# Kernel optimization log

Hardware: AMD Instinct MI355X
Metric: run time of the kernel (lower is better)

Reference implementation:

```python
import jax, jax.numpy as jnp
import numpy as np

B, L, D = 32, 1024, 128

def setup_inputs() -> dict:
    key = jax.random.key(0)
    kq, kk, kv, ks = jax.random.split(key, 4)
    Q = jax.random.normal(kq, (B, L, D), dtype=jnp.float32)
    K = jax.random.normal(kk, (B, L, D), dtype=jnp.float32)
    V = jax.random.normal(kv, (B, L, D), dtype=jnp.float32)
    kg_sim = jax.random.uniform(ks, (B, L, L), dtype=jnp.float32)
    scale = jnp.float32(1.0 / np.sqrt(D))
    return {"Q": Q, "K": K, "V": V, "scale": scale, "kg_sim": kg_sim}

def reference(Q, K, V, scale, kg_sim):
    # attention = -1 * (Q @ K^T) * scale   [B, L, L]
    attn = -scale * jnp.einsum('bqd,bkd->bqk', Q, K)
    # attention = -softmax(attention, axis=-1)
    attn = -jax.nn.softmax(attn, axis=-1)
    # beta = softmax(attention * kg_sim, axis=-1)
    beta = jax.nn.softmax(attn * kg_sim, axis=-1)
    # context = beta @ V   [B, L, D]
    return jnp.einsum('bqk,bkd->bqd', beta, V)
```

## Files before the change

kernel.cpp:

```cpp
#include <hip/hip_runtime.h>
#include <hip/hip_bf16.h>

#define L 1024
#define D 128
#define NB 32
#define BQ 16

typedef __attribute__((ext_vector_type(8))) short short8;
typedef __attribute__((ext_vector_type(4))) short short4v;
typedef __attribute__((ext_vector_type(4))) float f32x4;

__device__ __forceinline__ unsigned short f2bf(float f) {
    union { float f; unsigned int u; } x; x.f = f;
    unsigned int r = x.u + 0x7FFF + ((x.u >> 16) & 1);
    return (unsigned short)(r >> 16);
}
__device__ __forceinline__ float bf2f(unsigned short u) {
    union { unsigned int u; float f; } x; x.u = ((unsigned int)u) << 16;
    return x.f;
}

__global__ void vt_kernel(const float* __restrict__ V, unsigned short* __restrict__ Vt) {
    __shared__ unsigned short t[32][40];
    int id = blockIdx.x;
    int b = id >> 7;
    int rest = id & 127;
    int kt = rest >> 2, dt = rest & 3;
    int k0 = kt * 32, d0 = dt * 32;
    int tid = threadIdx.x;

    int kl = tid >> 3, dl4 = (tid & 7) * 4;
    const float* src = V + (((size_t)b * L + (k0 + kl)) * D) + d0 + dl4;
    float4 v = *(const float4*)src;
    t[dl4 + 0][kl] = f2bf(v.x);
    t[dl4 + 1][kl] = f2bf(v.y);
    t[dl4 + 2][kl] = f2bf(v.z);
    t[dl4 + 3][kl] = f2bf(v.w);
    __syncthreads();

    int dl = tid >> 3, kl4 = (tid & 7) * 4;
    unsigned short* dst = Vt + (((size_t)b * D + (d0 + dl)) * L) + k0 + kl4;
    short4v o;
    o[0] = (short)t[dl][kl4 + 0];
    o[1] = (short)t[dl][kl4 + 1];
    o[2] = (short)t[dl][kl4 + 2];
    o[3] = (short)t[dl][kl4 + 3];
    *(short4v*)dst = o;
}

__global__ __launch_bounds__(256, 4)
void attn_kernel(const float* __restrict__ Q, const float* __restrict__ K,
                 const float* __restrict__ scale_p, const float* __restrict__ kg,
                 const unsigned short* __restrict__ Vt, float* __restrict__ out) {
    __shared__ unsigned short S16[BQ * 1032];
    __shared__ unsigned short QL[BQ * 136];
    __shared__ float row_scale[BQ];

    const int tid = threadIdx.x;
    const int b  = blockIdx.x >> 6;
    const int q0 = (blockIdx.x & 63) * BQ;
    const float nsc = -scale_p[0];

    {
        int row = tid >> 4;
        int c8  = (tid & 15) * 8;
        const float* qp = Q + (((size_t)b * L) + q0 + row) * D + c8;
        float4 v0 = *(const float4*)qp;
        float4 v1 = *(const float4*)(qp + 4);
        unsigned short* dst = &QL[row * 136 + c8];
        dst[0] = f2bf(v0.x * nsc); dst[1] = f2bf(v0.y * nsc);
        dst[2] = f2bf(v0.z * nsc); dst[3] = f2bf(v0.w * nsc);
        dst[4] = f2bf(v1.x * nsc); dst[5] = f2bf(v1.y * nsc);
        dst[6] = f2bf(v1.z * nsc); dst[7] = f2bf(v1.w * nsc);
    }
    __syncthreads();

    const int wave = tid >> 6, lane = tid & 63;
    const int lr = lane & 15;
    const int lg = lane >> 4;

    short8 aq[4];
#pragma unroll
    for (int kb = 0; kb < 4; kb++)
        aq[kb] = *(const short8*)&QL[lr * 136 + kb * 32 + lg * 8];

    for (int ct = wave; ct < 64; ct += 4) {
        const float* kp = K + (((size_t)b * L) + ct * 16 + lr) * D + lg * 8;
        f32x4 acc = {0.f, 0.f, 0.f, 0.f};
#pragma unroll
        for (int kb = 0; kb < 4; kb++) {
            float4 x0 = *(const float4*)(kp + kb * 32);
            float4 x1 = *(const float4*)(kp + kb * 32 + 4);
            short8 bf;
            bf[0] = (short)f2bf(x0.x); bf[1] = (short)f2bf(x0.y);
            bf[2] = (short)f2bf(x0.z); bf[3] = (short)f2bf(x0.w);
            bf[4] = (short)f2bf(x1.x); bf[5] = (short)f2bf(x1.y);
            bf[6] = (short)f2bf(x1.z); bf[7] = (short)f2bf(x1.w);
            acc = __builtin_amdgcn_mfma_f32_16x16x32_bf16(aq[kb], bf, acc, 0, 0, 0);
        }
#pragma unroll
        for (int r = 0; r < 4; r++)
            S16[(lg * 4 + r) * 1032 + ct * 16 + lr] = f2bf(acc[r]);
    }
    __syncthreads();

    const int row = tid >> 4, l = tid & 15;
    unsigned short* srow = &S16[row * 1032];

    float m1 = -3.4e38f;
#pragma unroll 4
    for (int j = 0; j < 16; j++) {
        short4v v = *(const short4v*)&srow[l * 4 + 64 * j];
        float a0 = bf2f((unsigned short)v[0]), a1 = bf2f((unsigned short)v[1]);
        float a2 = bf2f((unsigned short)v[2]), a3 = bf2f((unsigned short)v[3]);
        m1 = fmaxf(m1, fmaxf(fmaxf(a0, a1), fmaxf(a2, a3)));
    }
#pragma unroll
    for (int m = 1; m < 16; m <<= 1) m1 = fmaxf(m1, __shfl_xor(m1, m, 64));

    float z1 = 0.f;
#pragma unroll 4
    for (int j = 0; j < 16; j++) {
        unsigned short* p = &srow[l * 4 + 64 * j];
        short4v v = *(const short4v*)p;
        float e0 = __expf(bf2f((unsigned short)v[0]) - m1);
        float e1 = __expf(bf2f((unsigned short)v[1]) - m1);
        float e2 = __expf(bf2f((unsigned short)v[2]) - m1);
        float e3 = __expf(bf2f((unsigned short)v[3]) - m1);
        z1 += (e0 + e1) + (e2 + e3);
        short4v o; o[0] = (short)f2bf(e0); o[1] = (short)f2bf(e1);
        o[2] = (short)f2bf(e2); o[3] = (short)f2bf(e3);
        *(short4v*)p = o;
    }
#pragma unroll
    for (int m = 1; m < 16; m <<= 1) z1 += __shfl_xor(z1, m, 64);
    const float iz1 = 1.0f / z1;

    const float* kgrow = kg + (((size_t)b * L) + q0 + row) * L;
    float m2 = -3.4e38f;
#pragma unroll 4
    for (int j = 0; j < 16; j++) {
        int c = l * 4 + 64 * j;
        float4 g = *(const float4*)&kgrow[c];
        unsigned short* p = &srow[c];
        short4v v = *(const short4v*)p;
        float t0 = -(bf2f((unsigned short)v[0]) * iz1) * g.x;
        float t1 = -(bf2f((unsigned short)v[1]) * iz1) * g.y;
        float t2 = -(bf2f((unsigned short)v[2]) * iz1) * g.z;
        float t3 = -(bf2f((unsigned short)v[3]) * iz1) * g.w;
        m2 = fmaxf(m2, fmaxf(fmaxf(t0, t1), fmaxf(t2, t3)));
        short4v o; o[0] = (short)f2bf(t0); o[1] = (short)f2bf(t1);
        o[2] = (short)f2bf(t2); o[3] = (short)f2bf(t3);
        *(short4v*)p = o;
    }
#pragma unroll
    for (int m = 1; m < 16; m <<= 1) m2 = fmaxf(m2, __shfl_xor(m2, m, 64));

    float z2 = 0.f;
#pragma unroll 4
    for (int j = 0; j < 16; j++) {
        unsigned short* p = &srow[l * 4 + 64 * j];
        short4v v = *(const short4v*)p;
        float e0 = __expf(bf2f((unsigned short)v[0]) - m2);
        float e1 = __expf(bf2f((unsigned short)v[1]) - m2);
        float e2 = __expf(bf2f((unsigned short)v[2]) - m2);
        float e3 = __expf(bf2f((unsigned short)v[3]) - m2);
        z2 += (e0 + e1) + (e2 + e3);
        short4v o; o[0] = (short)f2bf(e0); o[1] = (short)f2bf(e1);
        o[2] = (short)f2bf(e2); o[3] = (short)f2bf(e3);
        *(short4v*)p = o;
    }
#pragma unroll
    for (int m = 1; m < 16; m <<= 1) z2 += __shfl_xor(z2, m, 64);
    if (l == 0) row_scale[row] = 1.0f / z2;
    __syncthreads();

    const int dt0 = wave * 2;
    f32x4 acc0 = {0.f, 0.f, 0.f, 0.f}, acc1 = {0.f, 0.f, 0.f, 0.f};
    const unsigned short* vt0 = Vt + (((size_t)b * D) + dt0 * 16 + lr) * L + lg * 8;
    const unsigned short* vt1 = vt0 + (size_t)16 * L;
    const unsigned short* brow = &S16[lr * 1032 + lg * 8];
#pragma unroll 8
    for (int kb = 0; kb < 32; kb++) {
        short8 a  = *(const short8*)(brow + kb * 32);
        short8 b0 = *(const short8*)(vt0 + kb * 32);
        short8 b1 = *(const short8*)(vt1 + kb * 32);
        acc0 = __builtin_amdgcn_mfma_f32_16x16x32_bf16(a, b0, acc0, 0, 0, 0);
        acc1 = __builtin_amdgcn_mfma_f32_16x16x32_bf16(a, b1, acc1, 0, 0, 0);
    }
    float* orow = out + (((size_t)b * L) + q0) * D;
#pragma unroll
    for (int r = 0; r < 4; r++) {
        int rq = lg * 4 + r;
        float rs = row_scale[rq];
        orow[(size_t)rq * D + dt0 * 16 + lr]       = acc0[r] * rs;
        orow[(size_t)rq * D + (dt0 + 1) * 16 + lr] = acc1[r] * rs;
    }
}

extern "C" void kernel_launch(void* const* d_in, const int* in_sizes, int n_in,
                              void* d_out, int out_size, void* d_ws, size_t ws_size,
                              hipStream_t stream) {
    const float* Q     = (const float*)d_in[0];
    const float* K     = (const float*)d_in[1];
    const float* V     = (const float*)d_in[2];
    const float* scale = (const float*)d_in[3];
    const float* kg    = (const float*)d_in[4];
    float* out = (float*)d_out;
    unsigned short* Vt = (unsigned short*)d_ws;

    vt_kernel<<<NB * 128, 256, 0, stream>>>(V, Vt);
    attn_kernel<<<NB * (L / BQ), 256, 0, stream>>>(Q, K, scale, kg, Vt, out);
}
```

Before: 367.8 us.

## Pre-convert K to bf16, prefetch kg into registers, fuse row max into QK

The prep kernel now also converts K to bf16 once into workspace, so the attention blocks stop re-reading and re-converting fp32 K 64 times per batch. Each attention block issues its kg_sim loads at kernel start into 16 float4 registers, which overlaps their latency with the QK phase. The first softmax's row max is computed from the MFMA accumulators and combined through a small shared array, which removes one LDS pass. The second-softmax intermediates stay in fp32 registers instead of round-tripping through bf16 LDS. The cost is about 64 extra VGPRs per thread, which may conflict with the launch_bounds occupancy target of 4 and cause spills or lower occupancy.

```diff
diff --git a/kernel.cpp b/kernel.cpp
--- a/kernel.cpp
+++ b/kernel.cpp
@@ -20,14 +20,28 @@
     return x.f;
 }
 
-__global__ void vt_kernel(const float* __restrict__ V, unsigned short* __restrict__ Vt) {
+__global__ void prep_kernel(const float* __restrict__ K, const float* __restrict__ V,
+                            unsigned short* __restrict__ Kb, unsigned short* __restrict__ Vt) {
     __shared__ unsigned short t[32][40];
     int id = blockIdx.x;
+    int tid = threadIdx.x;
+    if (id < 2048) {
+        size_t base = (size_t)id * 2048 + (size_t)tid * 8;
+        float4 a = *(const float4*)(K + base);
+        float4 c = *(const float4*)(K + base + 4);
+        short8 o;
+        o[0] = (short)f2bf(a.x); o[1] = (short)f2bf(a.y);
+        o[2] = (short)f2bf(a.z); o[3] = (short)f2bf(a.w);
+        o[4] = (short)f2bf(c.x); o[5] = (short)f2bf(c.y);
+        o[6] = (short)f2bf(c.z); o[7] = (short)f2bf(c.w);
+        *(short8*)(Kb + base) = o;
+        return;
+    }
+    id -= 2048;
     int b = id >> 7;
     int rest = id & 127;
     int kt = rest >> 2, dt = rest & 3;
     int k0 = kt * 32, d0 = dt * 32;
-    int tid = threadIdx.x;
 
     int kl = tid >> 3, dl4 = (tid & 7) * 4;
     const float* src = V + (((size_t)b * L + (k0 + kl)) * D) + d0 + dl4;
@@ -49,11 +63,12 @@
 }
 
 __global__ __launch_bounds__(256, 4)
-void attn_kernel(const float* __restrict__ Q, const float* __restrict__ K,
+void attn_kernel(const float* __restrict__ Q, const unsigned short* __restrict__ Kb,
                  const float* __restrict__ scale_p, const float* __restrict__ kg,
                  const unsigned short* __restrict__ Vt, float* __restrict__ out) {
     __shared__ unsigned short S16[BQ * 1032];
     __shared__ unsigned short QL[BQ * 136];
+    __shared__ float wmax[4 * BQ];
     __shared__ float row_scale[BQ];
 
     const int tid = threadIdx.x;
@@ -61,9 +76,15 @@
     const int q0 = (blockIdx.x & 63) * BQ;
     const float nsc = -scale_p[0];
 
+    const int row = tid >> 4, l = tid & 15;
+
+    const float* kgrow = kg + (((size_t)b * L) + q0 + row) * L + l * 4;
+    float4 kgv[16];
+#pragma unroll
+    for (int j = 0; j < 16; j++) kgv[j] = *(const float4*)(kgrow + 64 * j);
+
     {
-        int row = tid >> 4;
-        int c8  = (tid & 15) * 8;
+        int c8 = l * 8;
         const float* qp = Q + (((size_t)b * L) + q0 + row) * D + c8;
         float4 v0 = *(const float4*)qp;
         float4 v1 = *(const float4*)(qp + 4);
@@ -84,39 +105,37 @@
     for (int kb = 0; kb < 4; kb++)
         aq[kb] = *(const short8*)&QL[lr * 136 + kb * 32 + lg * 8];
 
-    for (int ct = wave; ct < 64; ct += 4) {
-        const float* kp = K + (((size_t)b * L) + ct * 16 + lr) * D + lg * 8;
+    f32x4 pm = {-3.4e38f, -3.4e38f, -3.4e38f, -3.4e38f};
+#pragma unroll 2
+    for (int i = 0; i < 16; i++) {
+        int ct = wave + i * 4;
+        const unsigned short* kp = Kb + (((size_t)b * L) + ct * 16 + lr) * D + lg * 8;
         f32x4 acc = {0.f, 0.f, 0.f, 0.f};
 #pragma unroll
         for (int kb = 0; kb < 4; kb++) {
-            float4 x0 = *(const float4*)(kp + kb * 32);
-            float4 x1 = *(const float4*)(kp + kb * 32 + 4);
-            short8 bf;
-            bf[0] = (short)f2bf(x0.x); bf[1] = (short)f2bf(x0.y);
-            bf[2] = (short)f2bf(x0.z); bf[3] = (short)f2bf(x0.w);
-            bf[4] = (short)f2bf(x1.x); bf[5] = (short)f2bf(x1.y);
-            bf[6] = (short)f2bf(x1.z); bf[7] = (short)f2bf(x1.w);
+            short8 bf = *(const short8*)(kp + kb * 32);
             acc = __builtin_amdgcn_mfma_f32_16x16x32_bf16(aq[kb], bf, acc, 0, 0, 0);
         }
 #pragma unroll
-        for (int r = 0; r < 4; r++)
+        for (int r = 0; r < 4; r++) {
             S16[(lg * 4 + r) * 1032 + ct * 16 + lr] = f2bf(acc[r]);
-    }
-    __syncthreads();
-
-    const int row = tid >> 4, l = tid & 15;
+            pm[r] = fmaxf(pm[r], acc[r]);
+        }
+    }
+#pragma unroll
+    for (int m = 1; m < 16; m <<= 1) {
+#pragma unroll
+        for (int r = 0; r < 4; r++) pm[r] = fmaxf(pm[r], __shfl_xor(pm[r], m, 64));
+    }
+    if (lr == 0) {
+#pragma unroll
+        for (int r = 0; r < 4; r++) wmax[wave * BQ + lg * 4 + r] = pm[r];
+    }
+    __syncthreads();
+
     unsigned short* srow = &S16[row * 1032];
-
-    float m1 = -3.4e38f;
-#pragma unroll 4
-    for (int j = 0; j < 16; j++) {
-        short4v v = *(const short4v*)&srow[l * 4 + 64 * j];
-        float a0 = bf2f((unsigned short)v[0]), a1 = bf2f((unsigned short)v[1]);
-        float a2 = bf2f((unsigned short)v[2]), a3 = bf2f((unsigned short)v[3]);
-        m1 = fmaxf(m1, fmaxf(fmaxf(a0, a1), fmaxf(a2, a3)));
-    }
-#pragma unroll
-    for (int m = 1; m < 16; m <<= 1) m1 = fmaxf(m1, __shfl_xor(m1, m, 64));
+    float m1 = fmaxf(fmaxf(wmax[row], wmax[BQ + row]),
+                     fmaxf(wmax[2 * BQ + row], wmax[3 * BQ + row]));
 
     float z1 = 0.f;
 #pragma unroll 4
@@ -136,39 +155,33 @@
     for (int m = 1; m < 16; m <<= 1) z1 += __shfl_xor(z1, m, 64);
     const float iz1 = 1.0f / z1;
 
-    const float* kgrow = kg + (((size_t)b * L) + q0 + row) * L;
     float m2 = -3.4e38f;
-#pragma unroll 4
+#pragma unroll
     for (int j = 0; j < 16; j++) {
-        int c = l * 4 + 64 * j;
-        float4 g = *(const float4*)&kgrow[c];
-        unsigned short* p = &srow[c];
-        short4v v = *(const short4v*)p;
+        short4v v = *(const short4v*)&srow[l * 4 + 64 * j];
+        float4 g = kgv[j];
         float t0 = -(bf2f((unsigned short)v[0]) * iz1) * g.x;
         float t1 = -(bf2f((unsigned short)v[1]) * iz1) * g.y;
         float t2 = -(bf2f((unsigned short)v[2]) * iz1) * g.z;
         float t3 = -(bf2f((unsigned short)v[3]) * iz1) * g.w;
         m2 = fmaxf(m2, fmaxf(fmaxf(t0, t1), fmaxf(t2, t3)));
-        short4v o; o[0] = (short)f2bf(t0); o[1] = (short)f2bf(t1);
-        o[2] = (short)f2bf(t2); o[3] = (short)f2bf(t3);
-        *(short4v*)p = o;
+        kgv[j] = make_float4(t0, t1, t2, t3);
     }
 #pragma unroll
     for (int m = 1; m < 16; m <<= 1) m2 = fmaxf(m2, __shfl_xor(m2, m, 64));
 
     float z2 = 0.f;
-#pragma unroll 4
+#pragma unroll
     for (int j = 0; j < 16; j++) {
-        unsigned short* p = &srow[l * 4 + 64 * j];
-        short4v v = *(const short4v*)p;
-        float e0 = __expf(bf2f((unsigned short)v[0]) - m2);
-        float e1 = __expf(bf2f((unsigned short)v[1]) - m2);
-        float e2 = __expf(bf2f((unsigned short)v[2]) - m2);
-        float e3 = __expf(bf2f((unsigned short)v[3]) - m2);
+        float4 t = kgv[j];
+        float e0 = __expf(t.x - m2);
+        float e1 = __expf(t.y - m2);
+        float e2 = __expf(t.z - m2);
+        float e3 = __expf(t.w - m2);
         z2 += (e0 + e1) + (e2 + e3);
         short4v o; o[0] = (short)f2bf(e0); o[1] = (short)f2bf(e1);
         o[2] = (short)f2bf(e2); o[3] = (short)f2bf(e3);
-        *(short4v*)p = o;
+        *(short4v*)&srow[l * 4 + 64 * j] = o;
     }
 #pragma unroll
     for (int m = 1; m < 16; m <<= 1) z2 += __shfl_xor(z2, m, 64);
@@ -208,7 +221,8 @@
     const float* kg    = (const float*)d_in[4];
     float* out = (float*)d_out;
     unsigned short* Vt = (unsigned short*)d_ws;
-
-    vt_kernel<<<NB * 128, 256, 0, stream>>>(V, Vt);
-    attn_kernel<<<NB * (L / BQ), 256, 0, stream>>>(Q, K, scale, kg, Vt, out);
-}
+    unsigned short* Kb = (unsigned short*)d_ws + (size_t)NB * D * L;
+
+    prep_kernel<<<6144, 256, 0, stream>>>(K, V, Kb, Vt);
+    attn_kernel<<<NB * (L / BQ), 256, 0, stream>>>(Q, Kb, scale, kg, Vt, out);
+}
```

After: 339.3 us. 7.7% less time.
